# Performance work log

Hardware: AMD Instinct MI355X
Metric: run time of the kernel (lower is better)

Reference implementation:

```python
import jax, jax.numpy as jnp
import numpy as np

N, L, D = 16, 3136, 768  # batch, H*W (perfect square: 56*56), hidden_size
H = 8                    # head_count
K = D                    # key_channels
V = D // 2               # value_channels
M = 4 * D                # mlp_dim
EPS = 1e-6


def setup_inputs() -> dict:
    key = jax.random.key(0)
    ks = jax.random.split(key, 12)
    s = lambda d: 1.0 / np.sqrt(d)
    return {
        "x": jax.random.normal(ks[0], (N, L, D), dtype=jnp.float32),
        "ln1_g": jnp.ones((D,), jnp.float32),
        "ln1_b": jnp.zeros((D,), jnp.float32),
        # 1x1 conv weights stored as [out_ch, in_ch]
        "Wk": jax.random.normal(ks[1], (K, D), jnp.float32) * s(D),
        "bk": jnp.zeros((K,), jnp.float32),
        "Wq": jax.random.normal(ks[2], (K, D), jnp.float32) * s(D),
        "bq": jnp.zeros((K,), jnp.float32),
        "Wv": jax.random.normal(ks[3], (V, D), jnp.float32) * s(D),
        "bv": jnp.zeros((V,), jnp.float32),
        "Wr": jax.random.normal(ks[4], (D, V), jnp.float32) * s(V),
        "br": jnp.zeros((D,), jnp.float32),
        "ln2_g": jnp.ones((D,), jnp.float32),
        "ln2_b": jnp.zeros((D,), jnp.float32),
        # Linear weights stored as [out, in] (torch convention)
        "W1": jax.random.normal(ks[5], (M, D), jnp.float32) * s(D),
        "b1": jax.random.normal(ks[6], (M,), jnp.float32) * 1e-6,
        "W2": jax.random.normal(ks[7], (D, M), jnp.float32) * s(M),
        "b2": jax.random.normal(ks[8], (D,), jnp.float32) * 1e-6,
    }


def _layernorm(x, g, b):
    m = jnp.mean(x, axis=-1, keepdims=True)
    v = jnp.mean(jnp.square(x - m), axis=-1, keepdims=True)
    return (x - m) * jax.lax.rsqrt(v + EPS) * g + b


def _efficient_attention(x, Wk, bk, Wq, bq, Wv, bv, Wr, br):
    n, l, d = x.shape
    hk, hv = K // H, V // H
    # faithful to torch: input_.view(n, D, h, w) is a raw reshape, not transpose
    xf = x.reshape(n, d, l)  # [n, D, L]
    keys = jnp.einsum('kd,ndl->nkl', Wk, xf) + bk[None, :, None]
    queries = jnp.einsum('kd,ndl->nkl', Wq, xf) + bq[None, :, None]
    values = jnp.einsum('vd,ndl->nvl', Wv, xf) + bv[None, :, None]
    kh = jax.nn.softmax(keys.reshape(n, H, hk, l), axis=3)     # softmax over spatial
    qh = jax.nn.softmax(queries.reshape(n, H, hk, l), axis=2)  # softmax over head channels
    vh = values.reshape(n, H, hv, l)
    context = jnp.einsum('nhkl,nhvl->nhkv', kh, vh)            # [n,H,hk,hv]
    att = jnp.einsum('nhkv,nhkl->nhvl', context, qh)           # [n,H,hv,L]
    agg = att.reshape(n, V, l)
    out = jnp.einsum('dv,nvl->ndl', Wr, agg) + br[None, :, None]
    return out.reshape(n, l, d)  # faithful raw reshape back


def reference(x, ln1_g, ln1_b, Wk, bk, Wq, bq, Wv, bv, Wr, br,
              ln2_g, ln2_b, W1, b1, W2, b2):
    h = x
    y = _layernorm(x, ln1_g, ln1_b)
    y = _efficient_attention(y, Wk, bk, Wq, bq, Wv, bv, Wr, br)
    x = y + h
    h = x
    y = _layernorm(x, ln2_g, ln2_b)
    y = jax.nn.gelu(y @ W1.T + b1, approximate=False)
    y = y @ W2.T + b2
    return y + h
```

## Files before the change

kernel.cpp:

```cpp
#include <hip/hip_runtime.h>
#include <hip/hip_bf16.h>

using bf16 = __hip_bfloat16;
typedef __attribute__((ext_vector_type(8))) short short8;
typedef __attribute__((ext_vector_type(4))) short short4v;
typedef __attribute__((ext_vector_type(4))) float f32x4;

__device__ __forceinline__ float bfbits2f(unsigned short h) {
    unsigned v = (unsigned)h << 16;
    return __uint_as_float(v);
}

__device__ __forceinline__ void gload16(const void* g, void* l) {
    __builtin_amdgcn_global_load_lds(
        (const __attribute__((address_space(1))) unsigned int*)g,
        (__attribute__((address_space(3))) unsigned int*)l, 16, 0, 0);
}

__device__ __forceinline__ float gelu_fast(float x) {
    float x2 = x * x;
    float u = x * __builtin_fmaf(0.07135481f, x2, 1.59576912f);
    float e = __expf(u);
    return x - x * __builtin_amdgcn_rcpf(e + 1.0f);
}

__device__ __forceinline__ float blk_sum3(float v, float* red) {
#pragma unroll
    for (int o = 32; o > 0; o >>= 1) v += __shfl_down(v, o, 64);
    int wv = threadIdx.x >> 6;
    __syncthreads();
    if ((threadIdx.x & 63) == 0) red[wv] = v;
    __syncthreads();
    return red[0] + red[1] + red[2];
}

__global__ __launch_bounds__(192) void ln_f32(const float* __restrict__ x,
                                              const float* __restrict__ g,
                                              const float* __restrict__ b,
                                              bf16* __restrict__ y) {
    __shared__ float red[3];
    size_t base = (size_t)blockIdx.x * 768;
    int t = threadIdx.x;
    float4 v = *(const float4*)&x[base + t * 4];
    float s = blk_sum3(v.x + v.y + v.z + v.w, red);
    float mean = s * (1.0f / 768.0f);
    float d0 = v.x - mean, d1 = v.y - mean, d2 = v.z - mean, d3 = v.w - mean;
    float sq = blk_sum3(d0 * d0 + d1 * d1 + d2 * d2 + d3 * d3, red);
    float rstd = rsqrtf(sq * (1.0f / 768.0f) + 1e-6f);
    float4 gv = *(const float4*)&g[t * 4];
    float4 bv = *(const float4*)&b[t * 4];
    short4v o;
    o[0] = (short)__bfloat16_as_ushort(__float2bfloat16(d0 * rstd * gv.x + bv.x));
    o[1] = (short)__bfloat16_as_ushort(__float2bfloat16(d1 * rstd * gv.y + bv.y));
    o[2] = (short)__bfloat16_as_ushort(__float2bfloat16(d2 * rstd * gv.z + bv.z));
    o[3] = (short)__bfloat16_as_ushort(__float2bfloat16(d3 * rstd * gv.w + bv.w));
    *(short4v*)&((unsigned short*)y)[base + t * 4] = o;
}

__global__ __launch_bounds__(192) void ln_bf(const bf16* __restrict__ x,
                                             const float* __restrict__ g,
                                             const float* __restrict__ b,
                                             bf16* __restrict__ y) {
    __shared__ float red[3];
    size_t base = (size_t)blockIdx.x * 768;
    int t = threadIdx.x;
    short4v w = *(const short4v*)&((const unsigned short*)x)[base + t * 4];
    float v0 = bfbits2f((unsigned short)w[0]), v1 = bfbits2f((unsigned short)w[1]);
    float v2 = bfbits2f((unsigned short)w[2]), v3 = bfbits2f((unsigned short)w[3]);
    float s = blk_sum3(v0 + v1 + v2 + v3, red);
    float mean = s * (1.0f / 768.0f);
    float d0 = v0 - mean, d1 = v1 - mean, d2 = v2 - mean, d3 = v3 - mean;
    float sq = blk_sum3(d0 * d0 + d1 * d1 + d2 * d2 + d3 * d3, red);
    float rstd = rsqrtf(sq * (1.0f / 768.0f) + 1e-6f);
    float4 gv = *(const float4*)&g[t * 4];
    float4 bv = *(const float4*)&b[t * 4];
    short4v o;
    o[0] = (short)__bfloat16_as_ushort(__float2bfloat16(d0 * rstd * gv.x + bv.x));
    o[1] = (short)__bfloat16_as_ushort(__float2bfloat16(d1 * rstd * gv.y + bv.y));
    o[2] = (short)__bfloat16_as_ushort(__float2bfloat16(d2 * rstd * gv.z + bv.z));
    o[3] = (short)__bfloat16_as_ushort(__float2bfloat16(d3 * rstd * gv.w + bv.w));
    *(short4v*)&((unsigned short*)y)[base + t * 4] = o;
}

__global__ __launch_bounds__(256) void prep(
    const float* __restrict__ Wk, const float* __restrict__ Wq,
    const float* __restrict__ Wv, const float* __restrict__ Wr,
    const float* __restrict__ W1, const float* __restrict__ W2,
    const float* __restrict__ bk, const float* __restrict__ bq,
    const float* __restrict__ bv,
    bf16* __restrict__ Wkqv, bf16* __restrict__ Wrb,
    bf16* __restrict__ W1b, bf16* __restrict__ W2b, float* __restrict__ bkqv) {
    int i = blockIdx.x * 256 + threadIdx.x;
    const int nKQV = 2048 * 768, nWr = 768 * 384, nW1 = 3072 * 768, nW2 = 768 * 3072;
    if (i < nKQV) {
        int r = i / 768;
        float v = 0.f;
        if (r < 768) v = Wk[i];
        else if (r < 1536) v = Wq[i - 768 * 768];
        else if (r < 1920) v = Wv[i - 1536 * 768];
        Wkqv[i] = __float2bfloat16(v);
        return;
    }
    i -= nKQV;
    if (i < nWr) { Wrb[i] = __float2bfloat16(Wr[i]); return; }
    i -= nWr;
    if (i < nW1) { W1b[i] = __float2bfloat16(W1[i]); return; }
    i -= nW1;
    if (i < nW2) { W2b[i] = __float2bfloat16(W2[i]); return; }
    i -= nW2;
    if (i < 1920) bkqv[i] = (i < 768) ? bk[i] : (i < 1536 ? bq[i - 768] : bv[i - 1536]);
}

__global__ __launch_bounds__(256) void transp_k(const bf16* __restrict__ Y,
                                                bf16* __restrict__ Xt) {
    __shared__ unsigned short tile[64][65];
    const size_t LD = (size_t)768 * 3136;
    int n = blockIdx.z;
    int l0 = blockIdx.x * 64, d0 = blockIdx.y * 64;
    const unsigned short* Yp = (const unsigned short*)Y + (size_t)n * LD;
    unsigned short* Xp = (unsigned short*)Xt + (size_t)n * LD;
    int t = threadIdx.x;
#pragma unroll
    for (int j = 0; j < 2; j++) {
        int e = t + 256 * j;
        int dd = e >> 3, lg = (e & 7) * 8;
        short8 v = *(const short8*)&Yp[(size_t)(d0 + dd) * 3136 + l0 + lg];
#pragma unroll
        for (int u = 0; u < 8; u++) tile[dd][lg + u] = (unsigned short)v[u];
    }
    __syncthreads();
#pragma unroll
    for (int j = 0; j < 2; j++) {
        int e = t + 256 * j;
        int ll = e >> 3, dg = (e & 7) * 8;
        short8 v;
#pragma unroll
        for (int u = 0; u < 8; u++) v[u] = (short)tile[dg + u][ll];
        *(short8*)&Xp[(size_t)(l0 + ll) * 768 + d0 + dg] = v;
    }
}

template <int MODE>
__global__ __launch_bounds__(512, 2) void gemm256(
    const bf16* __restrict__ A, const bf16* __restrict__ B,
    const float* __restrict__ bias, const void* __restrict__ resid,
    void* __restrict__ C0, void* __restrict__ C1, void* __restrict__ C2,
    int M, int N, int K) {
    extern __shared__ char smem[];
    const int tid = threadIdx.x;
    const int lane = tid & 63, wave = tid >> 6;

    const int nbn = gridDim.x;
    const int nwg = nbn * gridDim.y;
    const int orig = blockIdx.y * nbn + blockIdx.x;
    const int qq = nwg >> 3, rm = nwg & 7;
    const int xcd = orig & 7, pos = orig >> 3;
    const int work = (xcd < rm ? xcd * (qq + 1) : rm * (qq + 1) + (xcd - rm) * qq) + pos;
    const int bn = work % nbn, bm = work / nbn;

    const int wm = (wave >> 2) * 128, wn = (wave & 3) * 64;
    const int frow = lane & 15, fsb = lane >> 4, fxr = frow & 7;
    const int srow = lane >> 3, sslot = (lane & 7) ^ srow;
    const size_t rowB = (size_t)K * 2;
    const char* Ap = (const char*)A + (size_t)(bm * 256 + wave * 32 + srow) * rowB + sslot * 16;
    const char* Bp = (const char*)B + (size_t)(bn * 256 + wave * 32 + srow) * rowB + sslot * 16;
    char* lA = smem + wave * 32 * 128;
    char* lB = smem + 32768 + wave * 32 * 128;

    f32x4 acc[8][4];
#pragma unroll
    for (int mi = 0; mi < 8; mi++)
#pragma unroll
        for (int ni = 0; ni < 4; ni++)
#pragma unroll
            for (int r = 0; r < 4; r++) acc[mi][ni][r] = 0.0f;

    auto stage = [&](int kt, int p) {
#pragma unroll
        for (int c = 0; c < 4; c++) {
            gload16(Ap + (size_t)c * 8 * rowB + (size_t)kt * 2, lA + p * 65536 + c * 1024);
            gload16(Bp + (size_t)c * 8 * rowB + (size_t)kt * 2, lB + p * 65536 + c * 1024);
        }
    };
    const int nt = K >> 6;
    stage(0, 0);
    stage(64, 1);
    for (int t = 0; t < nt; ++t) {
        if (t == nt - 1)
            asm volatile("s_waitcnt vmcnt(0)" ::: "memory");
        else
            asm volatile("s_waitcnt vmcnt(8)" ::: "memory");
        __builtin_amdgcn_s_barrier();
        asm volatile("" ::: "memory");
        const bf16* As = (const bf16*)(smem + (t & 1) * 65536);
        const bf16* Bs = (const bf16*)(smem + (t & 1) * 65536 + 32768);
#pragma unroll
        for (int k2 = 0; k2 < 2; k2++) {
            const int ko = ((k2 * 4 + fsb) ^ fxr) << 3;
            short8 bfv[4];
#pragma unroll
            for (int ni = 0; ni < 4; ni++)
                bfv[ni] = *(const short8*)&Bs[(wn + ni * 16 + frow) * 64 + ko];
#pragma unroll
            for (int half = 0; half < 2; half++) {
                short8 af[4];
#pragma unroll
                for (int i = 0; i < 4; i++)
                    af[i] = *(const short8*)&As[(wm + (half * 4 + i) * 16 + frow) * 64 + ko];
#pragma unroll
                for (int i = 0; i < 4; i++)
#pragma unroll
                    for (int ni = 0; ni < 4; ni++)
                        acc[half * 4 + i][ni] = __builtin_amdgcn_mfma_f32_16x16x32_bf16(
                            af[i], bfv[ni], acc[half * 4 + i][ni], 0, 0, 0);
            }
        }
        asm volatile("" ::: "memory");
        __builtin_amdgcn_s_barrier();
        if (t + 2 < nt) stage((t + 2) * 64, t & 1);
    }

    const unsigned short* Rb = (const unsigned short*)resid;
#pragma unroll
    for (int mi = 0; mi < 8; mi++)
#pragma unroll
        for (int ni = 0; ni < 4; ni++)
#pragma unroll
            for (int r = 0; r < 4; r++) {
                int row = bm * 256 + wm + mi * 16 + fsb * 4 + r;
                int col = bn * 256 + wn + ni * 16 + frow;
                float v = acc[mi][ni][r];
                if (MODE == 0) {
                    if (col < 1920) {
                        float o = v + bias[col];
                        if (col < 768)
                            ((bf16*)C0)[(size_t)row * 768 + col] = __float2bfloat16(o);
                        else if (col < 1536)
                            ((bf16*)C1)[(size_t)row * 768 + col - 768] = __float2bfloat16(o);
                        else
                            ((bf16*)C2)[(size_t)row * 384 + col - 1536] = __float2bfloat16(o);
                    }
                } else if (MODE == 2) {
                    ((bf16*)C0)[(size_t)row * N + col] =
                        __float2bfloat16(gelu_fast(v + bias[col]));
                } else {
                    size_t idx = (size_t)row * N + col;
                    ((float*)C0)[idx] = v + bias[col] + bfbits2f(Rb[idx]);
                }
            }
}

template <int MODE>
__global__ __launch_bounds__(256) void gemm_nk(
    const bf16* __restrict__ A, const bf16* __restrict__ B,
    const float* __restrict__ bias, const void* __restrict__ resid,
    void* __restrict__ C0, int M, int N, int K, long sB, long sC, long sR) {
    __shared__ bf16 As[128 * 64];
    __shared__ bf16 Bs[128 * 64];
    const int tid = threadIdx.x;
    const int lane = tid & 63, wave = tid >> 6;
    const int nbn = gridDim.x;
    const int nwg = nbn * gridDim.y;
    const int orig = blockIdx.y * nbn + blockIdx.x;
    const int qq = nwg >> 3, rm = nwg & 7;
    const int xcd = orig & 7, pos = orig >> 3;
    const int work = (xcd < rm ? xcd * (qq + 1) : rm * (qq + 1) + (xcd - rm) * qq) + pos;
    const int bn = work % nbn, bm = work / nbn;
    const int bz = blockIdx.z;

    const int wm = (wave >> 1) * 64, wn = (wave & 1) * 64;
    const int frow = lane & 15, fsb = lane >> 4, fxr = frow & 7;
    const int srow = lane >> 3, sslot = (lane & 7) ^ srow;
    const size_t rowB = (size_t)K * 2;
    const char* Ap = (const char*)A +
        ((size_t)bm * 128 + wave * 32 + srow) * rowB + (size_t)sslot * 16;
    const char* Bp = (const char*)(B + (size_t)bz * sB) +
        ((size_t)bn * 128 + wave * 32 + srow) * rowB + (size_t)sslot * 16;

    f32x4 acc[4][4];
#pragma unroll
    for (int mi = 0; mi < 4; mi++)
#pragma unroll
        for (int ni = 0; ni < 4; ni++)
#pragma unroll
            for (int r = 0; r < 4; r++) acc[mi][ni][r] = 0.0f;

    for (int kt = 0; kt < K; kt += 64) {
#pragma unroll
        for (int c = 0; c < 4; c++) {
            gload16(Ap + (size_t)c * 8 * rowB + (size_t)kt * 2, &As[(wave * 4 + c) * 512]);
            gload16(Bp + (size_t)c * 8 * rowB + (size_t)kt * 2, &Bs[(wave * 4 + c) * 512]);
        }
        __syncthreads();
#pragma unroll
        for (int k2 = 0; k2 < 2; k2++) {
            short8 af[4], bfv[4];
#pragma unroll
            for (int mi = 0; mi < 4; mi++) {
                int r = wm + mi * 16 + frow;
                af[mi] = *(const short8*)&As[r * 64 + (((k2 * 4 + fsb) ^ fxr) << 3)];
            }
#pragma unroll
            for (int ni = 0; ni < 4; ni++) {
                int r = wn + ni * 16 + frow;
                bfv[ni] = *(const short8*)&Bs[r * 64 + (((k2 * 4 + fsb) ^ fxr) << 3)];
            }
#pragma unroll
            for (int mi = 0; mi < 4; mi++)
#pragma unroll
                for (int ni = 0; ni < 4; ni++)
                    acc[mi][ni] = __builtin_amdgcn_mfma_f32_16x16x32_bf16(
                        af[mi], bfv[ni], acc[mi][ni], 0, 0, 0);
        }
        __syncthreads();
    }

    const float* Rf = (const float*)resid + (size_t)bz * sR;
#pragma unroll
    for (int mi = 0; mi < 4; mi++)
#pragma unroll
        for (int ni = 0; ni < 4; ni++)
#pragma unroll
            for (int r = 0; r < 4; r++) {
                int row = bm * 128 + wm + mi * 16 + (fsb << 2) + r;
                int col = bn * 128 + wn + ni * 16 + frow;
                if (col < N) {
                    float v = acc[mi][ni][r];
                    size_t idx = (size_t)row * N + col;
                    bf16* Cb = (bf16*)C0 + (size_t)bz * sC;
                    Cb[idx] = __float2bfloat16(v + bias[row] + Rf[idx]);
                }
            }
}

__global__ __launch_bounds__(256) void context_k(const bf16* __restrict__ Kt,
                                                 const bf16* __restrict__ Vt,
                                                 float* __restrict__ ctx,
                                                 float* __restrict__ Sf) {
    __shared__ float ks[32][96];
    __shared__ float vs[32][48];
    int nh = blockIdx.y;
    int n = nh >> 3, h = nh & 7;
    int t = threadIdx.x;
    const unsigned short* kp = (const unsigned short*)Kt;
    const unsigned short* vp = (const unsigned short*)Vt;
    int a = t >> 4, bq = t & 15;
    float acc[6][3];
    float sacc[6];
#pragma unroll
    for (int i = 0; i < 6; i++) {
        sacc[i] = 0.f;
#pragma unroll
        for (int j = 0; j < 3; j++) acc[i][j] = 0.f;
    }
    int l0 = blockIdx.x * 448;
    for (int ls = l0; ls < l0 + 448; ls += 32) {
        __syncthreads();
#pragma unroll
        for (int j = 0; j < 6; j++) {
            int e = t + 256 * j;
            int row = e / 48, cp = e % 48;
            unsigned u = *(const unsigned*)&kp[((size_t)(n * 3136 + ls + row)) * 768 + h * 96 + cp * 2];
            ks[row][cp * 2] = __expf(bfbits2f((unsigned short)(u & 0xffff)));
            ks[row][cp * 2 + 1] = __expf(bfbits2f((unsigned short)(u >> 16)));
        }
#pragma unroll
        for (int j = 0; j < 3; j++) {
            int e = t + 256 * j;
            int row = e / 24, cp = e % 24;
            unsigned u = *(const unsigned*)&vp[((size_t)(n * 3136 + ls + row)) * 384 + h * 48 + cp * 2];
            vs[row][cp * 2] = bfbits2f((unsigned short)(u & 0xffff));
            vs[row][cp * 2 + 1] = bfbits2f((unsigned short)(u >> 16));
        }
        __syncthreads();
        for (int ll = 0; ll < 32; ll++) {
            float kv[6], vv[3];
#pragma unroll
            for (int i = 0; i < 6; i++) { kv[i] = ks[ll][a * 6 + i]; sacc[i] += kv[i]; }
#pragma unroll
            for (int j = 0; j < 3; j++) vv[j] = vs[ll][bq * 3 + j];
#pragma unroll
            for (int i = 0; i < 6; i++)
#pragma unroll
                for (int j = 0; j < 3; j++) acc[i][j] += kv[i] * vv[j];
        }
    }
    float* cb = ctx + (size_t)nh * 4608;
#pragma unroll
    for (int i = 0; i < 6; i++) {
#pragma unroll
        for (int j = 0; j < 3; j++)
            atomicAdd(&cb[(a * 6 + i) * 48 + bq * 3 + j], acc[i][j]);
        if (bq == 0) atomicAdd(&Sf[(size_t)nh * 96 + a * 6 + i], sacc[i]);
    }
}

__global__ __launch_bounds__(256) void att_k(const float* __restrict__ ctx,
                                             const float* __restrict__ Sf,
                                             const bf16* __restrict__ Qt,
                                             bf16* __restrict__ att) {
    __shared__ float cs[4608];
    __shared__ float sinv[96];
    int nh = blockIdx.y;
    int n = nh >> 3, h = nh & 7;
    if (threadIdx.x < 96)
        sinv[threadIdx.x] = 1.0f / Sf[(size_t)nh * 96 + threadIdx.x];
    __syncthreads();
    for (int j = threadIdx.x; j < 4608; j += 256)
        cs[j] = ctx[(size_t)nh * 4608 + j] * sinv[j / 48];
    __syncthreads();
    int l = blockIdx.x * 256 + threadIdx.x;
    if (l >= 3136) return;
    const unsigned short* qp = (const unsigned short*)Qt + ((size_t)(n * 3136 + l)) * 768 + h * 96;
    float qv[96];
    float s = 0.f;
#pragma unroll
    for (int j = 0; j < 12; j++) {
        short8 w = *(const short8*)&qp[j * 8];
#pragma unroll
        for (int x = 0; x < 8; x++) {
            float e = __expf(bfbits2f((unsigned short)w[x]));
            qv[j * 8 + x] = e;
            s += e;
        }
    }
    float inv = 1.0f / s;
    unsigned short ov[48];
#pragma unroll
    for (int vb = 0; vb < 12; vb++) {
        f32x4 acc4;
        acc4[0] = acc4[1] = acc4[2] = acc4[3] = 0.f;
        for (int k = 0; k < 96; k++) {
            f32x4 c4 = *(const f32x4*)&cs[k * 48 + vb * 4];
            float q = qv[k];
#pragma unroll
            for (int x = 0; x < 4; x++) acc4[x] += c4[x] * q;
        }
#pragma unroll
        for (int x = 0; x < 4; x++)
            ov[vb * 4 + x] = __bfloat16_as_ushort(__float2bfloat16(acc4[x] * inv));
    }
    unsigned short* op = (unsigned short*)att + ((size_t)n * 3200 + l) * 384 + h * 48;
#pragma unroll
    for (int j = 0; j < 6; j++) *(short8*)&op[j * 8] = *(short8*)&ov[j * 8];
}

extern "C" void kernel_launch(void* const* d_in, const int* in_sizes, int n_in,
                              void* d_out, int out_size, void* d_ws, size_t ws_size,
                              hipStream_t stream) {
    (void)in_sizes; (void)n_in; (void)out_size; (void)ws_size;
    const float* x     = (const float*)d_in[0];
    const float* ln1_g = (const float*)d_in[1];
    const float* ln1_b = (const float*)d_in[2];
    const float* Wk    = (const float*)d_in[3];
    const float* bk    = (const float*)d_in[4];
    const float* Wq    = (const float*)d_in[5];
    const float* bq    = (const float*)d_in[6];
    const float* Wv    = (const float*)d_in[7];
    const float* bv    = (const float*)d_in[8];
    const float* Wr    = (const float*)d_in[9];
    const float* br    = (const float*)d_in[10];
    const float* ln2_g = (const float*)d_in[11];
    const float* ln2_b = (const float*)d_in[12];
    const float* W1    = (const float*)d_in[13];
    const float* b1    = (const float*)d_in[14];
    const float* W2    = (const float*)d_in[15];
    const float* b2    = (const float*)d_in[16];

    const int Nb = 16, L = 3136;
    const size_t LD = (size_t)L * 768;
    const size_t sz77 = (size_t)50176 * 768 * 2;

    char* w = (char*)d_ws;
    size_t off = 0;
    auto alloc = [&](size_t bytes) {
        char* p = w + off;
        off = (off + bytes + 255) & ~(size_t)255;
        return p;
    };
    bf16* Ybf  = (bf16*)alloc(sz77);
    bf16* Xt   = (bf16*)alloc(sz77);
    bf16* Kt   = (bf16*)alloc(sz77);
    bf16* Qt   = (bf16*)alloc(sz77);
    bf16* Vt   = (bf16*)alloc((size_t)50176 * 384 * 2);
    bf16* attb = (bf16*)alloc((size_t)16 * 3200 * 384 * 2);
    bf16* x1   = (bf16*)alloc(sz77);
    bf16* Wkqv_bf = (bf16*)alloc((size_t)2048 * 768 * 2);
    bf16* Wr_bf = (bf16*)alloc((size_t)768 * 384 * 2);
    bf16* W1_bf = (bf16*)alloc((size_t)3072 * 768 * 2);
    bf16* W2_bf = (bf16*)alloc((size_t)768 * 3072 * 2);
    float* bkqv = (float*)alloc((size_t)1920 * 4);
    float* ctx = (float*)Xt;
    float* Sf  = (float*)((char*)Xt + 4718592);
    bf16* Hbf  = Ybf;
    bf16* Y2bf = Vt;

    prep<<<25736, 256, 0, stream>>>(Wk, Wq, Wv, Wr, W1, W2, bk, bq, bv,
                                    Wkqv_bf, Wr_bf, W1_bf, W2_bf, bkqv);

    hipFuncSetAttribute((const void*)gemm256<0>,
                        hipFuncAttributeMaxDynamicSharedMemorySize, 131072);
    hipFuncSetAttribute((const void*)gemm256<2>,
                        hipFuncAttributeMaxDynamicSharedMemorySize, 131072);
    hipFuncSetAttribute((const void*)gemm256<3>,
                        hipFuncAttributeMaxDynamicSharedMemorySize, 131072);

    ln_f32<<<Nb * L, 192, 0, stream>>>(x, ln1_g, ln1_b, Ybf);
    transp_k<<<dim3(49, 12, 16), 256, 0, stream>>>(Ybf, Xt);

    gemm256<0><<<dim3(8, 196), 512, 131072, stream>>>(
        Xt, Wkqv_bf, bkqv, nullptr, Kt, Qt, Vt, 50176, 2048, 768);

    hipMemsetAsync(ctx, 0, 4718592 + 49152, stream);
    context_k<<<dim3(7, 128), 256, 0, stream>>>(Kt, Vt, ctx, Sf);
    att_k<<<dim3(13, 128), 256, 0, stream>>>(ctx, Sf, Qt, attb);

    gemm_nk<1><<<dim3(25, 6, 16), 256, 0, stream>>>(
        Wr_bf, attb, br, x, x1, 768, 3136, 384,
        (long)3200 * 384, (long)LD, (long)LD);

    ln_bf<<<Nb * L, 192, 0, stream>>>(x1, ln2_g, ln2_b, Y2bf);

    gemm256<2><<<dim3(12, 196), 512, 131072, stream>>>(
        Y2bf, W1_bf, b1, nullptr, Hbf, nullptr, nullptr, 50176, 3072, 768);
    gemm256<3><<<dim3(3, 196), 512, 131072, stream>>>(
        Hbf, W2_bf, b2, x1, d_out, nullptr, nullptr, 50176, 768, 3072);
}
```

Baseline: 1.381 ms.

## Split GEMM k-tile into half-slabs with finer-grained staged loads and MFMA priority

The 256x256 bf16 GEMM mainloop now splits each 64-wide k-tile into two 32-wide LDS slabs with a new swizzle. Global-to-LDS loads for A and B of the next slabs are interleaved between four MFMA phases, each separated by barriers. s_setprio raises wave priority during MFMA bursts. The aim is to overlap memory traffic with compute more evenly and cut LDS bank conflicts. In exchange it adds many more barriers per iteration and relies on delicate vmcnt accounting.

```diff
diff --git a/kernel.cpp b/kernel.cpp
--- a/kernel.cpp
+++ b/kernel.cpp
@@ -159,13 +159,13 @@
     const int bn = work % nbn, bm = work / nbn;
 
     const int wm = (wave >> 2) * 128, wn = (wave & 3) * 64;
-    const int frow = lane & 15, fsb = lane >> 4, fxr = frow & 7;
-    const int srow = lane >> 3, sslot = (lane & 7) ^ srow;
+    const int frow = lane & 15, fsb = lane >> 4;
+    const int rslot = (fsb ^ ((frow >> 1) & 3)) * 16;
+    const int srowS = lane >> 2;
+    const int sslotS = (lane & 3) ^ ((lane >> 3) & 3);
     const size_t rowB = (size_t)K * 2;
-    const char* Ap = (const char*)A + (size_t)(bm * 256 + wave * 32 + srow) * rowB + sslot * 16;
-    const char* Bp = (const char*)B + (size_t)(bn * 256 + wave * 32 + srow) * rowB + sslot * 16;
-    char* lA = smem + wave * 32 * 128;
-    char* lB = smem + 32768 + wave * 32 * 128;
+    const char* ApS = (const char*)A + (size_t)(bm * 256 + wave * 32 + srowS) * rowB + sslotS * 16;
+    const char* BpS = (const char*)B + (size_t)(bn * 256 + wave * 32 + srowS) * rowB + sslotS * 16;
 
     f32x4 acc[8][4];
 #pragma unroll
@@ -175,49 +175,115 @@
 #pragma unroll
             for (int r = 0; r < 4; r++) acc[mi][ni][r] = 0.0f;
 
-    auto stage = [&](int kt, int p) {
-#pragma unroll
-        for (int c = 0; c < 4; c++) {
-            gload16(Ap + (size_t)c * 8 * rowB + (size_t)kt * 2, lA + p * 65536 + c * 1024);
-            gload16(Bp + (size_t)c * 8 * rowB + (size_t)kt * 2, lB + p * 65536 + c * 1024);
-        }
+    auto stA = [&](int t, int k2) {
+        char* d = smem + (t & 1) * 65536 + k2 * 16384 + wave * 2048;
+        const char* s = ApS + (size_t)t * 128 + k2 * 64;
+        gload16(s, d);
+        gload16(s + (size_t)16 * rowB, d + 1024);
     };
+    auto stB = [&](int t, int k2) {
+        char* d = smem + (t & 1) * 65536 + 32768 + k2 * 16384 + wave * 2048;
+        const char* s = BpS + (size_t)t * 128 + k2 * 64;
+        gload16(s, d);
+        gload16(s + (size_t)16 * rowB, d + 1024);
+    };
+
     const int nt = K >> 6;
-    stage(0, 0);
-    stage(64, 1);
+    stA(0, 0); stB(0, 0); stA(0, 1); stB(0, 1);
+    stA(1, 0); stB(1, 0);
+    asm volatile("s_waitcnt vmcnt(8)" ::: "memory");
+    __builtin_amdgcn_s_barrier();
+    asm volatile("" ::: "memory");
+
     for (int t = 0; t < nt; ++t) {
+        const char* base = smem + (t & 1) * 65536;
+        short8 bfv[4], af[4];
+#pragma unroll
+        for (int ni = 0; ni < 4; ni++)
+            bfv[ni] = *(const short8*)(base + 32768 + (wn + ni * 16 + frow) * 64 + rslot);
+#pragma unroll
+        for (int i = 0; i < 4; i++)
+            af[i] = *(const short8*)(base + (wm + i * 16 + frow) * 64 + rslot);
+        if (t + 1 < nt) stA(t + 1, 1);
+        asm volatile("" ::: "memory");
+        __builtin_amdgcn_s_barrier();
+        asm volatile("" ::: "memory");
+        __builtin_amdgcn_s_setprio(1);
+#pragma unroll
+        for (int i = 0; i < 4; i++)
+#pragma unroll
+            for (int ni = 0; ni < 4; ni++)
+                acc[i][ni] = __builtin_amdgcn_mfma_f32_16x16x32_bf16(
+                    af[i], bfv[ni], acc[i][ni], 0, 0, 0);
+        __builtin_amdgcn_s_setprio(0);
+        asm volatile("" ::: "memory");
+        __builtin_amdgcn_s_barrier();
+        asm volatile("" ::: "memory");
+#pragma unroll
+        for (int i = 0; i < 4; i++)
+            af[i] = *(const short8*)(base + (wm + (4 + i) * 16 + frow) * 64 + rslot);
+        if (t + 1 < nt) stB(t + 1, 1);
+        asm volatile("" ::: "memory");
+        __builtin_amdgcn_s_barrier();
+        asm volatile("" ::: "memory");
+        __builtin_amdgcn_s_setprio(1);
+#pragma unroll
+        for (int i = 0; i < 4; i++)
+#pragma unroll
+            for (int ni = 0; ni < 4; ni++)
+                acc[4 + i][ni] = __builtin_amdgcn_mfma_f32_16x16x32_bf16(
+                    af[i], bfv[ni], acc[4 + i][ni], 0, 0, 0);
+        __builtin_amdgcn_s_setprio(0);
         if (t == nt - 1)
             asm volatile("s_waitcnt vmcnt(0)" ::: "memory");
         else
             asm volatile("s_waitcnt vmcnt(8)" ::: "memory");
         __builtin_amdgcn_s_barrier();
         asm volatile("" ::: "memory");
-        const bf16* As = (const bf16*)(smem + (t & 1) * 65536);
-        const bf16* Bs = (const bf16*)(smem + (t & 1) * 65536 + 32768);
-#pragma unroll
-        for (int k2 = 0; k2 < 2; k2++) {
-            const int ko = ((k2 * 4 + fsb) ^ fxr) << 3;
-            short8 bfv[4];
+#pragma unroll
+        for (int ni = 0; ni < 4; ni++)
+            bfv[ni] = *(const short8*)(base + 32768 + 16384 + (wn + ni * 16 + frow) * 64 + rslot);
+#pragma unroll
+        for (int i = 0; i < 4; i++)
+            af[i] = *(const short8*)(base + 16384 + (wm + i * 16 + frow) * 64 + rslot);
+        if (t + 2 < nt) stA(t + 2, 0);
+        asm volatile("" ::: "memory");
+        __builtin_amdgcn_s_barrier();
+        asm volatile("" ::: "memory");
+        __builtin_amdgcn_s_setprio(1);
+#pragma unroll
+        for (int i = 0; i < 4; i++)
 #pragma unroll
             for (int ni = 0; ni < 4; ni++)
-                bfv[ni] = *(const short8*)&Bs[(wn + ni * 16 + frow) * 64 + ko];
-#pragma unroll
-            for (int half = 0; half < 2; half++) {
-                short8 af[4];
-#pragma unroll
-                for (int i = 0; i < 4; i++)
-                    af[i] = *(const short8*)&As[(wm + (half * 4 + i) * 16 + frow) * 64 + ko];
-#pragma unroll
-                for (int i = 0; i < 4; i++)
-#pragma unroll
-                    for (int ni = 0; ni < 4; ni++)
-                        acc[half * 4 + i][ni] = __builtin_amdgcn_mfma_f32_16x16x32_bf16(
-                            af[i], bfv[ni], acc[half * 4 + i][ni], 0, 0, 0);
-            }
-        }
-        asm volatile("" ::: "memory");
-        __builtin_amdgcn_s_barrier();
-        if (t + 2 < nt) stage((t + 2) * 64, t & 1);
+                acc[i][ni] = __builtin_amdgcn_mfma_f32_16x16x32_bf16(
+                    af[i], bfv[ni], acc[i][ni], 0, 0, 0);
+        __builtin_amdgcn_s_setprio(0);
+        asm volatile("" ::: "memory");
+        __builtin_amdgcn_s_barrier();
+        asm volatile("" ::: "memory");
+#pragma unroll
+        for (int i = 0; i < 4; i++)
+            af[i] = *(const short8*)(base + 16384 + (wm + (4 + i) * 16 + frow) * 64 + rslot);
+        if (t + 2 < nt) stB(t + 2, 0);
+        asm volatile("" ::: "memory");
+        __builtin_amdgcn_s_barrier();
+        asm volatile("" ::: "memory");
+        __builtin_amdgcn_s_setprio(1);
+#pragma unroll
+        for (int i = 0; i < 4; i++)
+#pragma unroll
+            for (int ni = 0; ni < 4; ni++)
+                acc[4 + i][ni] = __builtin_amdgcn_mfma_f32_16x16x32_bf16(
+                    af[i], bfv[ni], acc[4 + i][ni], 0, 0, 0);
+        __builtin_amdgcn_s_setprio(0);
+        if (t + 1 < nt) {
+            if (t + 1 == nt - 1)
+                asm volatile("s_waitcnt vmcnt(4)" ::: "memory");
+            else
+                asm volatile("s_waitcnt vmcnt(8)" ::: "memory");
+        }
+        __builtin_amdgcn_s_barrier();
+        asm volatile("" ::: "memory");
     }
 
     const unsigned short* Rb = (const unsigned short*)resid;
@@ -227,7 +293,7 @@
         for (int ni = 0; ni < 4; ni++)
 #pragma unroll
             for (int r = 0; r < 4; r++) {
-                int row = bm * 256 + wm + mi * 16 + fsb * 4 + r;
+                int row = bm * 256 + wm + mi * 16 + (lane >> 4) * 4 + r;
                 int col = bn * 256 + wn + ni * 16 + frow;
                 float v = acc[mi][ni][r];
                 if (MODE == 0) {
```

New measurement: 1.407 ms. Within noise of the previous version (+1.9%).
